# Kernel tuning notes

Hardware: AMD Instinct MI355X
Metric: run time of the kernel (lower is better)

The kernel has to match this reference:

```python
import jax, jax.numpy as jnp
import numpy as np

SHIFT = 1  # original module picks random(+1/-1) at init; fixed to +1 for determinism


def setup_inputs() -> dict:
    key = jax.random.key(0)
    k1, k2, k3 = jax.random.split(key, 3)
    x = jax.random.normal(k1, (1024, 1792, 14), dtype=jnp.float32)
    w1 = jax.random.normal(k2, (256, 2), dtype=jnp.float32)      # weights[0]
    w2 = jax.random.normal(k3, (128, 3, 256), dtype=jnp.float32)  # weights[1]
    return {"x": x, "w1": w1, "w2": w2}


def reference(x, w1, w2):
    m = 1024
    # Channels 1792 split as j(128) * l(14); H = 14. unfold((3,1), pad=(1,0)) is an
    # im2col over H with 3 taps; torch orders the unfolded channel dim as c*3+k,
    # so reshape (1024, 128, 14, 3, 14) puts taps k before spatial n -> permute to mjlnk.
    x4 = x.reshape(m, 128, 14, 14)                       # (m, j, l, h)
    xp = jnp.pad(x4, ((0, 0), (0, 0), (0, 0), (1, 1)))   # pad H by 1 each side
    win = jnp.stack([xp[..., 0:14], xp[..., 1:15], xp[..., 2:16]], axis=-1)  # (m,j,l,n,k)
    t4 = jnp.einsum('mjlnk,jki->mlni', win, w2)          # (1024, 14, 14, 256)
    t5 = jnp.einsum('mabj,ji->mabji', t4, w1)            # (1024, 14, 14, 256, 2) outer product
    t6 = jnp.roll(t5, SHIFT, axis=1)
    t6 = t6.transpose(0, 2, 3, 1, 4).reshape(m, 14, 256, 28)
    t6 = jnp.roll(t6, SHIFT, axis=3)
    t6 = t6.reshape(m, 14, 256, 14, 2).sum(axis=4)       # pairwise sum
    return t6.transpose(0, 2, 3, 1)                      # (1024, 256, 14, 14)
```

## Files before the change

kernel.cpp:

```cpp
#include <hip/hip_runtime.h>
#include <hip/hip_bf16.h>

typedef __bf16 bf16x8 __attribute__((ext_vector_type(8)));
typedef unsigned short u16x8 __attribute__((ext_vector_type(8)));
typedef float f32x4 __attribute__((ext_vector_type(4)));

__device__ __forceinline__ unsigned short f2bf(float f) {
    unsigned u = __builtin_bit_cast(unsigned, f);
    u += 0x7FFFu + ((u >> 16) & 1u);
    return (unsigned short)(u >> 16);
}
__device__ __forceinline__ float bf2f(unsigned short h) {
    unsigned u = ((unsigned)h) << 16;
    return __builtin_bit_cast(float, u);
}

__global__ void prep_w2(const float* __restrict__ w2, unsigned short* __restrict__ w2t) {
    int idx = blockIdx.x * 256 + threadIdx.x;
    if (idx < 128 * 3 * 256) {
        int i  = idx % 256;
        int jk = idx / 256;
        int j2 = jk / 3, k = jk % 3;
        w2t[i * 384 + k * 128 + j2] = f2bf(w2[idx]);
    }
}

__global__ __launch_bounds__(256, 2) void fused_conv_outer(
    const float* __restrict__ x, const float* __restrict__ w1,
    const unsigned short* __restrict__ w2t, float* __restrict__ out)
{
    __shared__ alignas(16) unsigned short xlds[196 * 136];
    __shared__ alignas(16) unsigned short cb[4 * 16 * 210];

    const int m    = blockIdx.x;
    const int tid  = threadIdx.x;
    const int wave = tid >> 6;
    const int lane = tid & 63;
    const int c16  = lane & 15;
    const int kgrp = lane >> 4;

    {
        const float* xm = x + (size_t)m * 25088;
        const int j2a = 2 * lane;
        const int rbase = wave * 48;
        const int rend  = (wave == 3) ? 52 : 48;
        for (int rr = 0; rr < rend; rr += 4) {
            const float4 v0 = *(const float4*)(xm + (size_t)j2a * 196 + rbase + rr);
            const float4 v1 = *(const float4*)(xm + (size_t)(j2a + 1) * 196 + rbase + rr);
            const float a0[4] = {v0.x, v0.y, v0.z, v0.w};
            const float a1[4] = {v1.x, v1.y, v1.z, v1.w};
#pragma unroll
            for (int i2 = 0; i2 < 4; ++i2) {
                unsigned pk = (unsigned)f2bf(a0[i2]) | ((unsigned)f2bf(a1[i2]) << 16);
                *(unsigned*)&xlds[(rbase + rr + i2) * 136 + j2a] = pk;
            }
        }
    }
    __syncthreads();

    unsigned short* cbw = &cb[wave * (16 * 210)];

#pragma unroll 1
    for (int nt = 0; nt < 4; ++nt) {
        const int ntile = wave * 4 + nt;
        const int col   = ntile * 16 + c16;

        bf16x8 Bf[12];
        {
            const unsigned short* bp = w2t + (size_t)col * 384 + kgrp * 8;
#pragma unroll
            for (int k = 0; k < 12; ++k)
                Bf[k] = __builtin_bit_cast(bf16x8, *(const u16x8*)(bp + k * 32));
        }

#pragma unroll 1
        for (int mt = 0; mt < 13; ++mt) {
            const int r0 = mt * 16 + c16;
            const int rc = (r0 < 196) ? r0 : 195;
            const int nn = rc % 14;

            bf16x8 Af[12];
#pragma unroll
            for (int k = 0; k < 12; ++k) {
                const int tap = k >> 2;
                const int h   = nn + tap - 1;
                if ((unsigned)h < 14u) {
                    Af[k] = __builtin_bit_cast(bf16x8,
                        *(const u16x8*)&xlds[(rc + tap - 1) * 136 + (k & 3) * 32 + kgrp * 8]);
                } else {
                    Af[k] = __builtin_bit_cast(bf16x8, (u16x8)(unsigned short)0);
                }
            }

            f32x4 acc = {0.f, 0.f, 0.f, 0.f};
#pragma unroll
            for (int k = 0; k < 12; ++k)
                acc = __builtin_amdgcn_mfma_f32_16x16x32_bf16(Af[k], Bf[k], acc, 0, 0, 0);

            const int rr0 = mt * 16 + kgrp * 4;
            if (rr0 < 196) {
                unsigned pk0 = (unsigned)f2bf(acc[0]) | ((unsigned)f2bf(acc[1]) << 16);
                unsigned pk1 = (unsigned)f2bf(acc[2]) | ((unsigned)f2bf(acc[3]) << 16);
                *(unsigned*)&cbw[c16 * 210 + rr0]     = pk0;
                *(unsigned*)&cbw[c16 * 210 + rr0 + 2] = pk1;
            }
        }

        int r1a[4], r2a[4], ea[4]; bool oka[4];
#pragma unroll
        for (int it = 0; it < 4; ++it) {
            int e = it * 64 + lane;
            oka[it] = (e < 196);
            int ec  = oka[it] ? e : 195;
            int cdx = ec / 14;
            int nn2 = ec - cdx * 14;
            r1a[it] = ((cdx + 13) % 14) * 14 + nn2;
            r2a[it] = ((cdx + 12) % 14) * 14 + nn2;
            ea[it]  = e;
        }
        float* outb = out + (size_t)m * 50176 + (size_t)ntile * 16 * 196;
#pragma unroll
        for (int c = 0; c < 16; ++c) {
            const float2 wv = *(const float2*)(w1 + (ntile * 16 + c) * 2);
            const unsigned short* cr = cbw + c * 210;
            float* op = outb + c * 196;
#pragma unroll
            for (int it = 0; it < 4; ++it) {
                if (oka[it]) {
                    float v = wv.x * bf2f(cr[r1a[it]]) + wv.y * bf2f(cr[r2a[it]]);
                    op[ea[it]] = v;
                }
            }
        }
    }
}

extern "C" void kernel_launch(void* const* d_in, const int* in_sizes, int n_in,
                              void* d_out, int out_size, void* d_ws, size_t ws_size,
                              hipStream_t stream) {
    const float* x  = (const float*)d_in[0];
    const float* w1 = (const float*)d_in[1];
    const float* w2 = (const float*)d_in[2];
    float* out = (float*)d_out;
    unsigned short* w2t = (unsigned short*)d_ws;

    prep_w2<<<384, 256, 0, stream>>>(w2, w2t);
    fused_conv_outer<<<1024, 256, 0, stream>>>(x, w1, w2t, out);
}
```

Before: 353.3 us.

## Split each batch item across two blocks and transpose conv buffer layout

```diff
diff --git a/kernel.cpp b/kernel.cpp
--- a/kernel.cpp
+++ b/kernel.cpp
@@ -1,5 +1,4 @@
 #include <hip/hip_runtime.h>
-#include <hip/hip_bf16.h>
 
 typedef __bf16 bf16x8 __attribute__((ext_vector_type(8)));
 typedef unsigned short u16x8 __attribute__((ext_vector_type(8)));
@@ -10,9 +9,11 @@
     u += 0x7FFFu + ((u >> 16) & 1u);
     return (unsigned short)(u >> 16);
 }
-__device__ __forceinline__ float bf2f(unsigned short h) {
-    unsigned u = ((unsigned)h) << 16;
-    return __builtin_bit_cast(float, u);
+__device__ __forceinline__ float bflo(unsigned w) {
+    return __builtin_bit_cast(float, w << 16);
+}
+__device__ __forceinline__ float bfhi(unsigned w) {
+    return __builtin_bit_cast(float, w & 0xFFFF0000u);
 }
 
 __global__ void prep_w2(const float* __restrict__ w2, unsigned short* __restrict__ w2t) {
@@ -25,14 +26,37 @@
     }
 }
 
-__global__ __launch_bounds__(256, 2) void fused_conv_outer(
+__device__ __forceinline__ void load14(const float* __restrict__ p, bool odd, float v[14]) {
+    if (odd) {
+        const float2 a  = *(const float2*)(p);
+        const float4 q0 = *(const float4*)(p + 2);
+        const float4 q1 = *(const float4*)(p + 6);
+        const float4 q2 = *(const float4*)(p + 10);
+        v[0]=a.x;  v[1]=a.y;
+        v[2]=q0.x; v[3]=q0.y; v[4]=q0.z;  v[5]=q0.w;
+        v[6]=q1.x; v[7]=q1.y; v[8]=q1.z;  v[9]=q1.w;
+        v[10]=q2.x; v[11]=q2.y; v[12]=q2.z; v[13]=q2.w;
+    } else {
+        const float4 q0 = *(const float4*)(p);
+        const float4 q1 = *(const float4*)(p + 4);
+        const float4 q2 = *(const float4*)(p + 8);
+        const float2 a  = *(const float2*)(p + 12);
+        v[0]=q0.x; v[1]=q0.y; v[2]=q0.z;  v[3]=q0.w;
+        v[4]=q1.x; v[5]=q1.y; v[6]=q1.z;  v[7]=q1.w;
+        v[8]=q2.x; v[9]=q2.y; v[10]=q2.z; v[11]=q2.w;
+        v[12]=a.x; v[13]=a.y;
+    }
+}
+
+__global__ __launch_bounds__(256, 3) void fused_conv_outer2(
     const float* __restrict__ x, const float* __restrict__ w1,
     const unsigned short* __restrict__ w2t, float* __restrict__ out)
 {
-    __shared__ alignas(16) unsigned short xlds[196 * 136];
-    __shared__ alignas(16) unsigned short cb[4 * 16 * 210];
+    __shared__ alignas(16) unsigned short xlds[112 * 136];
+    __shared__ alignas(16) unsigned short cb[4 * 112 * 18];
 
-    const int m    = blockIdx.x;
+    const int m    = blockIdx.x >> 1;
+    const int half = blockIdx.x & 1;
     const int tid  = threadIdx.x;
     const int wave = tid >> 6;
     const int lane = tid & 63;
@@ -42,42 +66,44 @@
     {
         const float* xm = x + (size_t)m * 25088;
         const int j2a = 2 * lane;
-        const int rbase = wave * 48;
-        const int rend  = (wave == 3) ? 52 : 48;
-        for (int rr = 0; rr < rend; rr += 4) {
-            const float4 v0 = *(const float4*)(xm + (size_t)j2a * 196 + rbase + rr);
-            const float4 v1 = *(const float4*)(xm + (size_t)(j2a + 1) * 196 + rbase + rr);
-            const float a0[4] = {v0.x, v0.y, v0.z, v0.w};
-            const float a1[4] = {v1.x, v1.y, v1.z, v1.w};
 #pragma unroll
-            for (int i2 = 0; i2 < 4; ++i2) {
-                unsigned pk = (unsigned)f2bf(a0[i2]) | ((unsigned)f2bf(a1[i2]) << 16);
-                *(unsigned*)&xlds[(rbase + rr + i2) * 136 + j2a] = pk;
+        for (int t = 0; t < 2; ++t) {
+            const int li = wave * 2 + t;
+            const int gl = half ? (6 + li) : (li < 7 ? li : 13);
+            float va[14], vb[14];
+            const float* b0 = xm + (size_t)j2a * 196 + gl * 14;
+            load14(b0,       (gl & 1) != 0, va);
+            load14(b0 + 196, (gl & 1) != 0, vb);
+            unsigned short* dst = &xlds[(li * 14) * 136 + j2a];
+#pragma unroll
+            for (int h = 0; h < 14; ++h) {
+                unsigned pk = (unsigned)f2bf(va[h]) | ((unsigned)f2bf(vb[h]) << 16);
+                *(unsigned*)&dst[h * 136] = pk;
             }
         }
     }
     __syncthreads();
 
-    unsigned short* cbw = &cb[wave * (16 * 210)];
+    unsigned short* cbw = &cb[wave * (112 * 18)];
+    float* outm = out + (size_t)m * 50176;
 
 #pragma unroll 1
     for (int nt = 0; nt < 4; ++nt) {
-        const int ntile = wave * 4 + nt;
-        const int col   = ntile * 16 + c16;
+        const int ntile   = wave * 4 + nt;
+        const int colbase = ntile * 16;
 
         bf16x8 Bf[12];
         {
-            const unsigned short* bp = w2t + (size_t)col * 384 + kgrp * 8;
+            const unsigned short* bp = w2t + (size_t)(colbase + c16) * 384 + kgrp * 8;
 #pragma unroll
             for (int k = 0; k < 12; ++k)
                 Bf[k] = __builtin_bit_cast(bf16x8, *(const u16x8*)(bp + k * 32));
         }
 
 #pragma unroll 1
-        for (int mt = 0; mt < 13; ++mt) {
+        for (int mt = 0; mt < 7; ++mt) {
             const int r0 = mt * 16 + c16;
-            const int rc = (r0 < 196) ? r0 : 195;
-            const int nn = rc % 14;
+            const int nn = r0 % 14;
 
             bf16x8 Af[12];
 #pragma unroll
@@ -86,7 +112,7 @@
                 const int h   = nn + tap - 1;
                 if ((unsigned)h < 14u) {
                     Af[k] = __builtin_bit_cast(bf16x8,
-                        *(const u16x8*)&xlds[(rc + tap - 1) * 136 + (k & 3) * 32 + kgrp * 8]);
+                        *(const u16x8*)&xlds[(r0 + tap - 1) * 136 + (k & 3) * 32 + kgrp * 8]);
                 } else {
                     Af[k] = __builtin_bit_cast(bf16x8, (u16x8)(unsigned short)0);
                 }
@@ -97,41 +123,44 @@
             for (int k = 0; k < 12; ++k)
                 acc = __builtin_amdgcn_mfma_f32_16x16x32_bf16(Af[k], Bf[k], acc, 0, 0, 0);
 
-            const int rr0 = mt * 16 + kgrp * 4;
-            if (rr0 < 196) {
-                unsigned pk0 = (unsigned)f2bf(acc[0]) | ((unsigned)f2bf(acc[1]) << 16);
-                unsigned pk1 = (unsigned)f2bf(acc[2]) | ((unsigned)f2bf(acc[3]) << 16);
-                *(unsigned*)&cbw[c16 * 210 + rr0]     = pk0;
-                *(unsigned*)&cbw[c16 * 210 + rr0 + 2] = pk1;
+            const int rrb = mt * 16 + kgrp * 4;
+#pragma unroll
+            for (int j = 0; j < 4; ++j)
+                cbw[(rrb + j) * 18 + c16] = f2bf(acc[j]);
+        }
+
+        asm volatile("s_waitcnt lgkmcnt(0)" ::: "memory");
+
+        float4 wv[8];
+#pragma unroll
+        for (int cp = 0; cp < 8; ++cp)
+            wv[cp] = *(const float4*)(w1 + (colbase + 2 * cp) * 2);
+
+        float* op = outm + (size_t)colbase * 196;
+#pragma unroll
+        for (int it = 0; it < 2; ++it) {
+            const int e   = it * 64 + lane;
+            const bool ok = (e < 98);
+            const int ec  = ok ? e : 97;
+            const int ci  = ec / 14;
+            const int n2  = ec - ci * 14;
+            int li1, li2, o;
+            if (half) { li1 = ci + 1; li2 = ci;            o = e + 112 - (ci == 6 ? 196 : 0); }
+            else      { li1 = ci;     li2 = (ci + 7) & 7;  o = e + 14; }
+            const int r1o = (li1 * 14 + n2) * 18;
+            const int r2o = (li2 * 14 + n2) * 18;
+#pragma unroll
+            for (int cp = 0; cp < 8; ++cp) {
+                const unsigned A = *(const unsigned*)&cbw[r1o + 2 * cp];
+                const unsigned B = *(const unsigned*)&cbw[r2o + 2 * cp];
+                if (ok) {
+                    op[(2 * cp) * 196 + o]     = wv[cp].x * bflo(A) + wv[cp].y * bflo(B);
+                    op[(2 * cp + 1) * 196 + o] = wv[cp].z * bfhi(A) + wv[cp].w * bfhi(B);
+                }
             }
         }
 
-        int r1a[4], r2a[4], ea[4]; bool oka[4];
-#pragma unroll
-        for (int it = 0; it < 4; ++it) {
-            int e = it * 64 + lane;
-            oka[it] = (e < 196);
-            int ec  = oka[it] ? e : 195;
-            int cdx = ec / 14;
-            int nn2 = ec - cdx * 14;
-            r1a[it] = ((cdx + 13) % 14) * 14 + nn2;
-            r2a[it] = ((cdx + 12) % 14) * 14 + nn2;
-            ea[it]  = e;
-        }
-        float* outb = out + (size_t)m * 50176 + (size_t)ntile * 16 * 196;
-#pragma unroll
-        for (int c = 0; c < 16; ++c) {
-            const float2 wv = *(const float2*)(w1 + (ntile * 16 + c) * 2);
-            const unsigned short* cr = cbw + c * 210;
-            float* op = outb + c * 196;
-#pragma unroll
-            for (int it = 0; it < 4; ++it) {
-                if (oka[it]) {
-                    float v = wv.x * bf2f(cr[r1a[it]]) + wv.y * bf2f(cr[r2a[it]]);
-                    op[ea[it]] = v;
-                }
-            }
-        }
+        asm volatile("" ::: "memory");
     }
 }
 
@@ -145,5 +174,5 @@
     unsigned short* w2t = (unsigned short*)d_ws;
 
     prep_w2<<<384, 256, 0, stream>>>(w2, w2t);
-    fused_conv_outer<<<1024, 256, 0, stream>>>(x, w1, w2t, out);
+    fused_conv_outer2<<<2048, 256, 0, stream>>>(x, w1, w2t, out);
 }
```

After: 361.9 us. 2.4% more time.
